# Performance work log

Hardware: AMD Instinct MI355X
Metric: run time of the kernel (lower is better)

## Reference

```python
import jax, jax.numpy as jnp
import numpy as np


def setup_inputs() -> dict:
    key = jax.random.key(0)
    ks = jax.random.split(key, 10)
    T, B, I, H, Z = 1024, 512, 128, 256, 1
    s = 0.1  # small init scale for stable recurrence
    return {
        "inputs": jax.random.normal(ks[0], (T, B, I), dtype=jnp.float32),
        "h0": jax.random.normal(ks[1], (B, H), dtype=jnp.float32) * s,
        "c0": jax.random.normal(ks[2], (B, H), dtype=jnp.float32) * s,
        "z0": jax.random.normal(ks[3], (B, Z), dtype=jnp.float32) * s,
        "W_ih": jax.random.normal(ks[4], (4 * H, I + Z), dtype=jnp.float32) * s,
        "W_hh": jax.random.normal(ks[5], (4 * H, H), dtype=jnp.float32) * s,
        "b_ih": jax.random.normal(ks[6], (4 * H,), dtype=jnp.float32) * s,
        "b_hh": jax.random.normal(ks[7], (4 * H,), dtype=jnp.float32) * s,
        "W_fc": jax.random.normal(ks[8], (Z, H), dtype=jnp.float32) * s,
        "b_fc": jax.random.normal(ks[9], (Z,), dtype=jnp.float32) * s,
    }


def reference(inputs, h0, c0, z0, W_ih, W_hh, b_ih, b_hh, W_fc, b_fc):
    def step(carry, x_t):
        h, c, z = carry
        xz = jnp.concatenate([x_t, z], axis=1)  # [B, I+Z]
        gates = xz @ W_ih.T + b_ih + h @ W_hh.T + b_hh  # [B, 4H]
        i_g, f_g, g_g, o_g = jnp.split(gates, 4, axis=1)  # torch gate order i,f,g,o
        i_g = jax.nn.sigmoid(i_g)
        f_g = jax.nn.sigmoid(f_g)
        g_g = jnp.tanh(g_g)
        o_g = jax.nn.sigmoid(o_g)
        c = f_g * c + i_g * g_g
        h = o_g * jnp.tanh(c)
        z = jnp.tanh(h @ W_fc.T + b_fc)  # [B, Z]
        return (h, c, z), z

    (h, c, _), outputs = jax.lax.scan(step, (h0, c0, z0), inputs)
    return outputs, h, c  # outputs: [T, B, Z]
```

## Files before the change

### kernel.cpp

```cpp
#include <hip/hip_runtime.h>
#include <hip/hip_bf16.h>
#include <stdint.h>

#define TT 1024
#define BB 512
#define II 128
#define HH 256
#define NKC 12
#define GSTR 132

typedef __attribute__((ext_vector_type(8))) short bf16x8;
typedef __attribute__((ext_vector_type(4))) float f32x4;
typedef __attribute__((ext_vector_type(4))) uint32_t u32x4;
typedef unsigned long long ull;

__device__ __forceinline__ float fsig(float x)  { return 1.0f / (1.0f + __expf(-x)); }
__device__ __forceinline__ float ftanh(float x) { return 1.0f - 2.0f / (__expf(2.0f * x) + 1.0f); }
__device__ __forceinline__ uint16_t f2bf(float f) {
    return __bfloat16_as_ushort(__float2bfloat16(f));
}
__device__ __forceinline__ float bf2lo(uint32_t w) { return __uint_as_float(w << 16); }
__device__ __forceinline__ float bf2hi(uint32_t w) { return __uint_as_float(w & 0xffff0000u); }

__global__ __launch_bounds__(512, 1) void lstm_kernel(
    const float* __restrict__ x,
    const float* __restrict__ h0, const float* __restrict__ c0,
    const float* __restrict__ z0,
    const float* __restrict__ W_ih, const float* __restrict__ W_hh,
    const float* __restrict__ b_ih, const float* __restrict__ b_hh,
    const float* __restrict__ Wfc, const float* __restrict__ bfc,
    ull* __restrict__ hbF, ull* __restrict__ hbS,
    float* __restrict__ out)
{
    __shared__ __align__(16) uint16_t a_sh[NKC * 4 * 16 * 8];
    __shared__ float g_sh[16 * GSTR];
    __shared__ float zp_sh[2][8][16];

    const int tid  = threadIdx.x;
    const int lane = tid & 63, wv = tid >> 6;
    const int bid  = blockIdx.x;
    const int mm   = bid >> 3;
    const int role = mm & 7, grp = (bid & 7) * 4 + (mm >> 3);
    const int b0   = grp * 16;
    const int arow = tid >> 5, auu = tid & 31;
    const int u_g  = role * 32 + auu;
    const int grole = wv, grow = lane & 15, gwq = lane >> 4;
    const int xrow = lane & 15, xoct = lane >> 4;

    bf16x8 wreg[NKC];
    {
        int lc = wv * 16 + (lane & 15);
        int col = (lc >> 5) * 256 + role * 32 + (lc & 31);
        #pragma unroll
        for (int kc = 0; kc < NKC; ++kc) {
            int k0 = kc * 32 + (lane >> 4) * 8;
            const float* src = (k0 < II) ? &W_ih[(size_t)col * (II + 1) + k0]
                                         : &W_hh[(size_t)col * HH + (k0 - II)];
            bf16x8 wv8;
            #pragma unroll
            for (int j = 0; j < 8; ++j) wv8[j] = (short)f2bf(src[j]);
            wreg[kc] = wv8;
        }
    }

    float bia[4], wzv[4];
    #pragma unroll
    for (int g = 0; g < 4; ++g) {
        int c = g * 256 + u_g;
        bia[g] = b_ih[c] + b_hh[c];
        wzv[g] = W_ih[(size_t)c * (II + 1) + II];
    }
    float wfc8[8];
    #pragma unroll
    for (int j = 0; j < 8; ++j) wfc8[j] = Wfc[grole * 32 + gwq * 8 + j];
    const float wfc  = Wfc[u_g];
    const float bfcs = bfc[0];
    const float z0r  = z0[b0 + arow];
    float c_r = c0[(size_t)(b0 + arow) * HH + u_g];

    {
        const float* hp = h0 + (size_t)(b0 + grow) * HH + grole * 32 + gwq * 8;
        uint4 pw;
        pw.x = (uint32_t)f2bf(hp[0]) | ((uint32_t)f2bf(hp[1]) << 16);
        pw.y = (uint32_t)f2bf(hp[2]) | ((uint32_t)f2bf(hp[3]) << 16);
        pw.z = (uint32_t)f2bf(hp[4]) | ((uint32_t)f2bf(hp[5]) << 16);
        pw.w = (uint32_t)f2bf(hp[6]) | ((uint32_t)f2bf(hp[7]) << 16);
        *(uint4*)&a_sh[(((4 + grole) * 4 + gwq) * 16 + grow) * 8] = pw;
    }
    float4 xA = make_float4(0.f, 0.f, 0.f, 0.f), xB = xA;
    if (wv < 4) {
        const float* xs = &x[(size_t)(b0 + xrow) * II + wv * 32 + xoct * 8];
        float4 u0 = *(const float4*)xs, u1 = *(const float4*)(xs + 4);
        ushort4 lo, hi;
        lo.x = f2bf(u0.x); lo.y = f2bf(u0.y); lo.z = f2bf(u0.z); lo.w = f2bf(u0.w);
        hi.x = f2bf(u1.x); hi.y = f2bf(u1.y); hi.z = f2bf(u1.z); hi.w = f2bf(u1.w);
        int de = ((wv * 4 + xoct) * 16 + xrow) * 8;
        *(ushort4*)&a_sh[de] = lo;
        *(ushort4*)&a_sh[de + 4] = hi;
        if (TT > 1) {
            const float* xs1 = &x[(size_t)(BB * II) + (size_t)(b0 + xrow) * II + wv * 32 + xoct * 8];
            xA = *(const float4*)xs1;
            xB = *(const float4*)(xs1 + 4);
        }
    }

    uint32_t strikes = 0;
    for (int t = 0; t <= TT; ++t) {
        if (wv < 4 && t > 0 && t < TT) {
            ushort4 lo, hi;
            lo.x = f2bf(xA.x); lo.y = f2bf(xA.y); lo.z = f2bf(xA.z); lo.w = f2bf(xA.w);
            hi.x = f2bf(xB.x); hi.y = f2bf(xB.y); hi.z = f2bf(xB.z); hi.w = f2bf(xB.w);
            int de = ((wv * 4 + xoct) * 16 + xrow) * 8;
            *(ushort4*)&a_sh[de] = lo;
            *(ushort4*)&a_sh[de + 4] = hi;
        }

        if (t > 0 && grole != role) {
            const int par = (t - 1) & 1;
            const size_t gidx = ((((size_t)par * 32 + grp) * 8 + grole) * 16 + grow) * 16
                              + gwq * 4;
            const ull* pF = hbF + gidx;
            const ull* pS = hbS + gidx;
            u32x4 a0, a1;
            uint32_t it = 0;
            const uint32_t cap = (strikes >= 4) ? 64u : (1u << 18);
            const uint32_t tt = (uint32_t)t;
            for (;;) {
                u32x4 f0, f1;
                asm volatile(
                    "global_load_dwordx4 %0, %2, off sc0\n\t"
                    "global_load_dwordx4 %1, %2, off offset:16 sc0\n\t"
                    "s_waitcnt vmcnt(0)"
                    : "=&v"(f0), "=&v"(f1) : "v"(pF) : "memory");
                if (min(min(f0.y, f0.w), min(f1.y, f1.w)) >= tt) { a0 = f0; a1 = f1; break; }
                ++it;
                if ((it & 3) != 0) { __builtin_amdgcn_s_sleep(1); continue; }
                u32x4 s0, s1;
                asm volatile(
                    "global_load_dwordx4 %0, %2, off sc0 sc1\n\t"
                    "global_load_dwordx4 %1, %2, off offset:16 sc0 sc1\n\t"
                    "s_waitcnt vmcnt(0)"
                    : "=&v"(s0), "=&v"(s1) : "v"(pS) : "memory");
                if (min(min(s0.y, s0.w), min(s1.y, s1.w)) >= tt) { a0 = s0; a1 = s1; break; }
                __builtin_amdgcn_s_sleep(1);
                if (it > cap) { ++strikes; a0 = s0; a1 = s1; break; }
            }
            uint32_t w0 = a0.x, w1 = a0.z, w2 = a1.x, w3 = a1.z;
            uint4 pw; pw.x = w0; pw.y = w1; pw.z = w2; pw.w = w3;
            *(uint4*)&a_sh[(((4 + grole) * 4 + gwq) * 16 + grow) * 8] = pw;
            float p = bf2lo(w0) * wfc8[0] + bf2hi(w0) * wfc8[1]
                    + bf2lo(w1) * wfc8[2] + bf2hi(w1) * wfc8[3]
                    + bf2lo(w2) * wfc8[4] + bf2hi(w2) * wfc8[5]
                    + bf2lo(w3) * wfc8[6] + bf2hi(w3) * wfc8[7];
            p += __shfl_xor(p, 16, 64);
            p += __shfl_xor(p, 32, 64);
            if (gwq == 0) zp_sh[t & 1][grole][grow] = p;
        }

        if (wv < 4 && t + 1 < TT) {
            const float* xs1 = &x[(size_t)(t + 1) * (BB * II)
                                  + (size_t)(b0 + xrow) * II + wv * 32 + xoct * 8];
            xA = *(const float4*)xs1;
            xB = *(const float4*)(xs1 + 4);
        }
        __syncthreads();

        if (t == TT) {
            if (role == 0 && tid < 16) {
                float s = bfcs;
                #pragma unroll
                for (int r = 0; r < 8; ++r) s += zp_sh[TT & 1][r][tid];
                out[(size_t)(TT - 1) * BB + b0 + tid] = ftanh(s);
            }
            break;
        }

        float zp_;
        if (t == 0) {
            zp_ = z0r;
        } else {
            float s = bfcs;
            #pragma unroll
            for (int r = 0; r < 8; ++r) s += zp_sh[t & 1][r][arow];
            zp_ = ftanh(s);
            if (role == 0 && auu == 0)
                out[(size_t)(t - 1) * BB + b0 + arow] = zp_;
        }

        f32x4 acc0 = {0.f, 0.f, 0.f, 0.f}, acc1 = {0.f, 0.f, 0.f, 0.f};
        #pragma unroll
        for (int kc = 0; kc < NKC; kc += 2) {
            bf16x8 a0 = *(const bf16x8*)&a_sh[((kc * 4 + (lane >> 4)) * 16 + (lane & 15)) * 8];
            acc0 = __builtin_amdgcn_mfma_f32_16x16x32_bf16(a0, wreg[kc], acc0, 0, 0, 0);
            bf16x8 a1 = *(const bf16x8*)&a_sh[(((kc + 1) * 4 + (lane >> 4)) * 16 + (lane & 15)) * 8];
            acc1 = __builtin_amdgcn_mfma_f32_16x16x32_bf16(a1, wreg[kc + 1], acc1, 0, 0, 0);
        }
        f32x4 acc = acc0 + acc1;
        {
            int r0 = (lane >> 4) * 4, cb = wv * 16 + (lane & 15);
            #pragma unroll
            for (int i = 0; i < 4; ++i) g_sh[(r0 + i) * GSTR + cb] = acc[i];
        }
        __syncthreads();

        float gi = g_sh[arow * GSTR +      auu] + bia[0] + wzv[0] * zp_;
        float gf = g_sh[arow * GSTR + 32 + auu] + bia[1] + wzv[1] * zp_;
        float gg = g_sh[arow * GSTR + 64 + auu] + bia[2] + wzv[2] * zp_;
        float go = g_sh[arow * GSTR + 96 + auu] + bia[3] + wzv[3] * zp_;
        float ig = fsig(gi), fg = fsig(gf), gc = ftanh(gg), og = fsig(go);
        float cn = fg * c_r + ig * gc;
        c_r = cn;
        float hn = og * ftanh(cn);

        uint32_t hb16 = f2bf(hn);
        uint32_t nb = __shfl_down(hb16, 1, 64);
        if (!(auu & 1)) {
            uint32_t word = hb16 | (nb << 16);
            *(uint32_t*)&a_sh[(((4 + role) * 4 + (auu >> 3)) * 16 + arow) * 8 + (auu & 7)]
                = word;
            ull q = ((ull)(uint32_t)(t + 1) << 32) | (ull)word;
            size_t o = ((((size_t)(t & 1) * 32 + grp) * 8 + role) * 16 + arow) * 16
                     + (auu >> 1);
            asm volatile("global_store_dwordx2 %0, %1, off sc0"
                         :: "v"(hbF + o), "v"(q) : "memory");
            asm volatile("global_store_dwordx2 %0, %1, off sc0 sc1"
                         :: "v"(hbS + o), "v"(q) : "memory");
        }
        float pz = hn * wfc;
        #pragma unroll
        for (int off = 16; off >= 1; off >>= 1) pz += __shfl_xor(pz, off, 32);
        if (auu == 0) zp_sh[(t + 1) & 1][role][arow] = pz;

        if (t == TT - 1) {
            size_t ho = (size_t)TT * BB + (size_t)(b0 + arow) * HH + u_g;
            out[ho] = hn;
            out[ho + (size_t)BB * HH] = cn;
        }
    }
}

extern "C" void kernel_launch(void* const* d_in, const int* in_sizes, int n_in,
                              void* d_out, int out_size, void* d_ws, size_t ws_size,
                              hipStream_t stream) {
    const float* x    = (const float*)d_in[0];
    const float* h0   = (const float*)d_in[1];
    const float* c0   = (const float*)d_in[2];
    const float* z0   = (const float*)d_in[3];
    const float* W_ih = (const float*)d_in[4];
    const float* W_hh = (const float*)d_in[5];
    const float* b_ih = (const float*)d_in[6];
    const float* b_hh = (const float*)d_in[7];
    const float* Wfc  = (const float*)d_in[8];
    const float* bfc  = (const float*)d_in[9];
    float* out = (float*)d_out;

    const size_t COPY = (size_t)2 * 32 * 8 * 16 * 16 * 8;
    if (ws_size >= 2 * COPY) {
        ull* hbF = (ull*)d_ws;
        ull* hbS = (ull*)((char*)d_ws + COPY);
        hipMemsetAsync(d_ws, 0, 2 * COPY, stream);
        lstm_kernel<<<256, 512, 0, stream>>>(x, h0, c0, z0, W_ih, W_hh, b_ih, b_hh,
                                             Wfc, bfc, hbF, hbS, out);
    } else {
        ull* hb = (ull*)d_ws;
        hipMemsetAsync(d_ws, 0, COPY, stream);
        lstm_kernel<<<256, 512, 0, stream>>>(x, h0, c0, z0, W_ih, W_hh, b_ih, b_hh,
                                             Wfc, bfc, hb, hb, out);
    }
}
```

Measured before the change: 2.512 ms.

## Use single system-coherent h buffer with two in-flight pipelined polling loads

Drops the dual fast/slow copies of the cross-block hidden-state exchange buffer and keeps only the system-scope (sc0 sc1) copy, so each producer issues one store instead of two. The consumer spin-wait now keeps two outstanding load pairs in flight and alternates between them using partial vmcnt waits, replacing the load-wait-sleep loop. Readiness is checked wavefront-wide with __all. This is meant to cut polling latency and store traffic on the per-timestep inter-block handoff. In exchange the poll loop no longer sleeps, which adds memory traffic while waiting, and the timeout cap is smaller.

```diff
diff --git a/kernel.cpp b/kernel.cpp
--- a/kernel.cpp
+++ b/kernel.cpp
@@ -29,8 +29,7 @@
     const float* __restrict__ W_ih, const float* __restrict__ W_hh,
     const float* __restrict__ b_ih, const float* __restrict__ b_hh,
     const float* __restrict__ Wfc, const float* __restrict__ bfc,
-    ull* __restrict__ hbF, ull* __restrict__ hbS,
-    float* __restrict__ out)
+    ull* __restrict__ hb, float* __restrict__ out)
 {
     __shared__ __align__(16) uint16_t a_sh[NKC * 4 * 16 * 8];
     __shared__ float g_sh[16 * GSTR];
@@ -119,32 +118,38 @@
             const int par = (t - 1) & 1;
             const size_t gidx = ((((size_t)par * 32 + grp) * 8 + grole) * 16 + grow) * 16
                               + gwq * 4;
-            const ull* pF = hbF + gidx;
-            const ull* pS = hbS + gidx;
-            u32x4 a0, a1;
+            const ull* pS = hb + gidx;
+            const uint32_t tt = (uint32_t)t;
+            const uint32_t cap = (strikes >= 4) ? 16u : (1u << 16);
+            u32x4 a0, a1, b0v, b1v;
+            int useB = 0;
+            asm volatile("global_load_dwordx4 %0, %2, off sc0 sc1\n\t"
+                         "global_load_dwordx4 %1, %2, off offset:16 sc0 sc1"
+                         : "=&v"(a0), "=&v"(a1) : "v"(pS) : "memory");
+            asm volatile("global_load_dwordx4 %0, %2, off sc0 sc1\n\t"
+                         "global_load_dwordx4 %1, %2, off offset:16 sc0 sc1"
+                         : "=&v"(b0v), "=&v"(b1v) : "v"(pS) : "memory");
             uint32_t it = 0;
-            const uint32_t cap = (strikes >= 4) ? 64u : (1u << 18);
-            const uint32_t tt = (uint32_t)t;
             for (;;) {
-                u32x4 f0, f1;
-                asm volatile(
-                    "global_load_dwordx4 %0, %2, off sc0\n\t"
-                    "global_load_dwordx4 %1, %2, off offset:16 sc0\n\t"
-                    "s_waitcnt vmcnt(0)"
-                    : "=&v"(f0), "=&v"(f1) : "v"(pF) : "memory");
-                if (min(min(f0.y, f0.w), min(f1.y, f1.w)) >= tt) { a0 = f0; a1 = f1; break; }
-                ++it;
-                if ((it & 3) != 0) { __builtin_amdgcn_s_sleep(1); continue; }
-                u32x4 s0, s1;
-                asm volatile(
-                    "global_load_dwordx4 %0, %2, off sc0 sc1\n\t"
-                    "global_load_dwordx4 %1, %2, off offset:16 sc0 sc1\n\t"
-                    "s_waitcnt vmcnt(0)"
-                    : "=&v"(s0), "=&v"(s1) : "v"(pS) : "memory");
-                if (min(min(s0.y, s0.w), min(s1.y, s1.w)) >= tt) { a0 = s0; a1 = s1; break; }
-                __builtin_amdgcn_s_sleep(1);
-                if (it > cap) { ++strikes; a0 = s0; a1 = s1; break; }
+                asm volatile("s_waitcnt vmcnt(2)" ::: "memory");
+                __builtin_amdgcn_sched_barrier(0);
+                uint32_t mn = min(min(a0.y, a0.w), min(a1.y, a1.w));
+                if (__all(mn >= tt)) break;
+                asm volatile("global_load_dwordx4 %0, %2, off sc0 sc1\n\t"
+                             "global_load_dwordx4 %1, %2, off offset:16 sc0 sc1"
+                             : "=&v"(a0), "=&v"(a1) : "v"(pS) : "memory");
+                asm volatile("s_waitcnt vmcnt(2)" ::: "memory");
+                __builtin_amdgcn_sched_barrier(0);
+                mn = min(min(b0v.y, b0v.w), min(b1v.y, b1v.w));
+                if (__all(mn >= tt)) { useB = 1; break; }
+                asm volatile("global_load_dwordx4 %0, %2, off sc0 sc1\n\t"
+                             "global_load_dwordx4 %1, %2, off offset:16 sc0 sc1"
+                             : "=&v"(b0v), "=&v"(b1v) : "v"(pS) : "memory");
+                if (++it > cap) { ++strikes; break; }
             }
+            asm volatile("s_waitcnt vmcnt(0)" ::: "memory");
+            __builtin_amdgcn_sched_barrier(0);
+            if (useB) { a0 = b0v; a1 = b1v; }
             uint32_t w0 = a0.x, w1 = a0.z, w2 = a1.x, w3 = a1.z;
             uint4 pw; pw.x = w0; pw.y = w1; pw.z = w2; pw.w = w3;
             *(uint4*)&a_sh[(((4 + grole) * 4 + gwq) * 16 + grow) * 8] = pw;
@@ -221,10 +226,8 @@
             ull q = ((ull)(uint32_t)(t + 1) << 32) | (ull)word;
             size_t o = ((((size_t)(t & 1) * 32 + grp) * 8 + role) * 16 + arow) * 16
                      + (auu >> 1);
-            asm volatile("global_store_dwordx2 %0, %1, off sc0"
-                         :: "v"(hbF + o), "v"(q) : "memory");
             asm volatile("global_store_dwordx2 %0, %1, off sc0 sc1"
-                         :: "v"(hbS + o), "v"(q) : "memory");
+                         :: "v"(hb + o), "v"(q) : "memory");
         }
         float pz = hn * wfc;
         #pragma unroll
@@ -255,16 +258,8 @@
     float* out = (float*)d_out;
 
     const size_t COPY = (size_t)2 * 32 * 8 * 16 * 16 * 8;
-    if (ws_size >= 2 * COPY) {
-        ull* hbF = (ull*)d_ws;
-        ull* hbS = (ull*)((char*)d_ws + COPY);
-        hipMemsetAsync(d_ws, 0, 2 * COPY, stream);
-        lstm_kernel<<<256, 512, 0, stream>>>(x, h0, c0, z0, W_ih, W_hh, b_ih, b_hh,
-                                             Wfc, bfc, hbF, hbS, out);
-    } else {
-        ull* hb = (ull*)d_ws;
-        hipMemsetAsync(d_ws, 0, COPY, stream);
-        lstm_kernel<<<256, 512, 0, stream>>>(x, h0, c0, z0, W_ih, W_hh, b_ih, b_hh,
-                                             Wfc, bfc, hb, hb, out);
-    }
+    ull* hb = (ull*)d_ws;
+    hipMemsetAsync(d_ws, 0, COPY, stream);
+    lstm_kernel<<<256, 512, 0, stream>>>(x, h0, c0, z0, W_ih, W_hh, b_ih, b_hh,
+                                         Wfc, bfc, hb, out);
 }
```

Result: slower. 3.023 ms (+20.3%).

## Probe XCC co-location at startup and pick polling strategy for hidden-state exchange

Applied to the files above, without the earlier changes.

At kernel start each block records its XCC id, and the eight blocks in a batch group check whether they all sit on the same XCC. If they do, the fast path polls the sc0-only buffer and checks the system-coherent copy less often (every 8th try instead of every 4th). If they do not, the kernel polls only the sc1 coherent buffer with no sleep and a smaller cap. This adds a startup handshake with a spin loop and an extra workspace region, and it relies on the hardware XCC_ID register and on the group's blocks being resident together.

```diff
diff --git a/kernel.cpp b/kernel.cpp
--- a/kernel.cpp
+++ b/kernel.cpp
@@ -30,11 +30,13 @@
     const float* __restrict__ b_ih, const float* __restrict__ b_hh,
     const float* __restrict__ Wfc, const float* __restrict__ bfc,
     ull* __restrict__ hbF, ull* __restrict__ hbS,
+    uint32_t* __restrict__ xbuf, int probe,
     float* __restrict__ out)
 {
     __shared__ __align__(16) uint16_t a_sh[NKC * 4 * 16 * 8];
     __shared__ float g_sh[16 * GSTR];
     __shared__ float zp_sh[2][8][16];
+    __shared__ int okshared;
 
     const int tid  = threadIdx.x;
     const int lane = tid & 63, wv = tid >> 6;
@@ -46,6 +48,28 @@
     const int u_g  = role * 32 + auu;
     const int grole = wv, grow = lane & 15, gwq = lane >> 4;
     const int xrow = lane & 15, xoct = lane >> 4;
+
+    uint32_t myxcc = 0;
+    asm volatile("s_getreg_b32 %0, hwreg(HW_REG_XCC_ID)" : "=s"(myxcc));
+    if (tid == 0) {
+        okshared = 1;
+        if (probe)
+            __hip_atomic_store(&xbuf[grp * 8 + role], 0xA5A50000u | (myxcc & 0xffu),
+                               __ATOMIC_RELAXED, __HIP_MEMORY_SCOPE_AGENT);
+    }
+    __syncthreads();
+    if (probe && tid < 8) {
+        uint32_t v = 0, it = 0;
+        do {
+            v = __hip_atomic_load(&xbuf[grp * 8 + tid], __ATOMIC_RELAXED,
+                                  __HIP_MEMORY_SCOPE_AGENT);
+            if (++it > (1u << 22)) break;
+        } while ((v & 0xffff0000u) != 0xA5A50000u);
+        bool good = ((v & 0xffff0000u) == 0xA5A50000u) && ((v & 0xffu) == (myxcc & 0xffu));
+        if (!good) okshared = 0;
+    }
+    __syncthreads();
+    const bool fastOK = probe && (okshared != 0);
 
     bf16x8 wreg[NKC];
     {
@@ -123,27 +147,41 @@
             const ull* pS = hbS + gidx;
             u32x4 a0, a1;
             uint32_t it = 0;
-            const uint32_t cap = (strikes >= 4) ? 64u : (1u << 18);
             const uint32_t tt = (uint32_t)t;
-            for (;;) {
-                u32x4 f0, f1;
-                asm volatile(
-                    "global_load_dwordx4 %0, %2, off sc0\n\t"
-                    "global_load_dwordx4 %1, %2, off offset:16 sc0\n\t"
-                    "s_waitcnt vmcnt(0)"
-                    : "=&v"(f0), "=&v"(f1) : "v"(pF) : "memory");
-                if (min(min(f0.y, f0.w), min(f1.y, f1.w)) >= tt) { a0 = f0; a1 = f1; break; }
-                ++it;
-                if ((it & 3) != 0) { __builtin_amdgcn_s_sleep(1); continue; }
-                u32x4 s0, s1;
-                asm volatile(
-                    "global_load_dwordx4 %0, %2, off sc0 sc1\n\t"
-                    "global_load_dwordx4 %1, %2, off offset:16 sc0 sc1\n\t"
-                    "s_waitcnt vmcnt(0)"
-                    : "=&v"(s0), "=&v"(s1) : "v"(pS) : "memory");
-                if (min(min(s0.y, s0.w), min(s1.y, s1.w)) >= tt) { a0 = s0; a1 = s1; break; }
-                __builtin_amdgcn_s_sleep(1);
-                if (it > cap) { ++strikes; a0 = s0; a1 = s1; break; }
+            if (fastOK) {
+                const uint32_t cap = (strikes >= 4) ? 64u : (1u << 18);
+                for (;;) {
+                    u32x4 f0, f1;
+                    asm volatile(
+                        "global_load_dwordx4 %0, %2, off sc0\n\t"
+                        "global_load_dwordx4 %1, %2, off offset:16 sc0\n\t"
+                        "s_waitcnt vmcnt(0)"
+                        : "=&v"(f0), "=&v"(f1) : "v"(pF) : "memory");
+                    if (min(min(f0.y, f0.w), min(f1.y, f1.w)) >= tt) { a0 = f0; a1 = f1; break; }
+                    ++it;
+                    if ((it & 7) != 0) { __builtin_amdgcn_s_sleep(1); continue; }
+                    u32x4 s0, s1;
+                    asm volatile(
+                        "global_load_dwordx4 %0, %2, off sc0 sc1\n\t"
+                        "global_load_dwordx4 %1, %2, off offset:16 sc0 sc1\n\t"
+                        "s_waitcnt vmcnt(0)"
+                        : "=&v"(s0), "=&v"(s1) : "v"(pS) : "memory");
+                    if (min(min(s0.y, s0.w), min(s1.y, s1.w)) >= tt) { a0 = s0; a1 = s1; break; }
+                    __builtin_amdgcn_s_sleep(1);
+                    if (it > cap) { ++strikes; a0 = s0; a1 = s1; break; }
+                }
+            } else {
+                const uint32_t cap = (strikes >= 4) ? 64u : (1u << 16);
+                for (;;) {
+                    u32x4 s0, s1;
+                    asm volatile(
+                        "global_load_dwordx4 %0, %2, off sc0 sc1\n\t"
+                        "global_load_dwordx4 %1, %2, off offset:16 sc0 sc1\n\t"
+                        "s_waitcnt vmcnt(0)"
+                        : "=&v"(s0), "=&v"(s1) : "v"(pS) : "memory");
+                    if (min(min(s0.y, s0.w), min(s1.y, s1.w)) >= tt) { a0 = s0; a1 = s1; break; }
+                    if (++it > cap) { ++strikes; a0 = s0; a1 = s1; break; }
+                }
             }
             uint32_t w0 = a0.x, w1 = a0.z, w2 = a1.x, w3 = a1.z;
             uint4 pw; pw.x = w0; pw.y = w1; pw.z = w2; pw.w = w3;
@@ -255,16 +293,17 @@
     float* out = (float*)d_out;
 
     const size_t COPY = (size_t)2 * 32 * 8 * 16 * 16 * 8;
-    if (ws_size >= 2 * COPY) {
+    if (ws_size >= 2 * COPY + 4096) {
         ull* hbF = (ull*)d_ws;
         ull* hbS = (ull*)((char*)d_ws + COPY);
-        hipMemsetAsync(d_ws, 0, 2 * COPY, stream);
+        uint32_t* xbuf = (uint32_t*)((char*)d_ws + 2 * COPY);
+        hipMemsetAsync(d_ws, 0, 2 * COPY + 4096, stream);
         lstm_kernel<<<256, 512, 0, stream>>>(x, h0, c0, z0, W_ih, W_hh, b_ih, b_hh,
-                                             Wfc, bfc, hbF, hbS, out);
+                                             Wfc, bfc, hbF, hbS, xbuf, 1, out);
     } else {
         ull* hb = (ull*)d_ws;
         hipMemsetAsync(d_ws, 0, COPY, stream);
         lstm_kernel<<<256, 512, 0, stream>>>(x, h0, c0, z0, W_ih, W_hh, b_ih, b_hh,
-                                             Wfc, bfc, hb, hb, out);
+                                             Wfc, bfc, hb, hb, (uint32_t*)d_ws, 0, out);
     }
 }
```

Measured after the change: 3.128 ms. 1.25x slower.
